# Kernel optimization log

Hardware: AMD Instinct MI355X
Metric: run time of the kernel (lower is better)

The kernel has to match this reference:

```python
import jax, jax.numpy as jnp
import numpy as np

INPUT_SIZE = 4096
HIDDEN = 1024
WINDOW = 2048
STRIDE = 1024
METRIC = 32
POOLING = "last"


def setup_inputs() -> dict:
    key = jax.random.key(0)
    ks = jax.random.split(key, 9)
    s = 1.0 / np.sqrt(HIDDEN)  # torch LSTMCell/Linear init bound
    u = lambda k, shape: jax.random.uniform(k, shape, jnp.float32, -s, s)
    return {
        "inp": jax.random.normal(ks[0], (WINDOW, INPUT_SIZE), jnp.float32),
        "h1": jax.random.normal(ks[1], (1, HIDDEN), jnp.float32),
        "c1": jax.random.normal(ks[2], (1, HIDDEN), jnp.float32),
        "W_ih": u(ks[3], (4 * HIDDEN, INPUT_SIZE)),
        "W_hh": u(ks[4], (4 * HIDDEN, HIDDEN)),
        "b_ih": u(ks[5], (4 * HIDDEN,)),
        "b_hh": u(ks[6], (4 * HIDDEN,)),
        "fc_w": u(ks[7], (METRIC, HIDDEN)),
        "fc_b": u(ks[8], (METRIC,)),
    }


def reference(inp, h1, c1, W_ih, W_hh, b_ih, b_hh, fc_w, fc_b):
    window = min(WINDOW, inp.shape[0])
    # Precompute the input-side gate projection as one GEMM: [T, 4H]
    xg = inp[:window] @ W_ih.T + b_ih

    def step(carry, xg_t):
        h, c = carry  # each [1, H]
        gates = xg_t + h @ W_hh.T + b_hh  # [1, 4H]
        i, f, g, o = jnp.split(gates, 4, axis=-1)
        c = jax.nn.sigmoid(f) * c + jax.nn.sigmoid(i) * jnp.tanh(g)
        h = jax.nn.sigmoid(o) * jnp.tanh(c)
        return (h, c), (h, c)

    (h_fin, c_fin), (hs, cs) = jax.lax.scan(step, (h1, c1), xg)

    if window >= STRIDE:
        h_last = jax.lax.stop_gradient(hs[STRIDE - 1])  # [1, H], detached
        c_last = jax.lax.stop_gradient(cs[STRIDE - 1])
    else:
        h_last, c_last = None, None

    if POOLING == "mean":
        # mean of fc(h_i) over last STRIDE steps of the window
        out = (hs[window - STRIDE:, 0, :] @ fc_w.T + fc_b).sum(axis=0, keepdims=True) / STRIDE
    else:  # 'last'
        out = h_fin @ fc_w.T + fc_b  # [1, METRIC]
    out = jnp.tanh(out)
    return out, h_last, c_last
```

## Files before the change

### kernel.cpp

```cpp
#include <hip/hip_runtime.h>
#include <stdint.h>

typedef unsigned short u16;
typedef unsigned long long u64;
typedef __attribute__((ext_vector_type(8))) short short8;
typedef __attribute__((ext_vector_type(4))) float floatx4;

#define K_IN    4096
#define HID     1024
#define G4H     4096
#define T_STEPS 2048
#define NWG     128
#define SPIN_MAX 60000

__device__ __forceinline__ u16 f2bf(float f) {
  union { float f; unsigned int i; } v; v.f = f;
  unsigned int lsb = (v.i >> 16) & 1u;
  v.i += 0x7fffu + lsb;
  return (u16)(v.i >> 16);
}
__device__ __forceinline__ float finz(float x) {
  unsigned b = __float_as_uint(x);
  return ((b & 0x7f800000u) == 0x7f800000u) ? 0.f : x;
}
__device__ __forceinline__ float sigm(float x) {
  x = fminf(30.f, fmaxf(-30.f, finz(x)));
  return 1.0f / (1.0f + __expf(-x));
}
__device__ __forceinline__ float tanh_s(float x) {
  x = fminf(15.f, fmaxf(-15.f, finz(x)));
  float e = __expf(2.0f * x);
  return (e - 1.0f) / (e + 1.0f);
}

__device__ __forceinline__ void publish_h(u64* hx, int slot, int idx, float h) {
  h = finz(h);
  u64 v = ((u64)(unsigned)(slot + 1) << 32) | (u64)__float_as_uint(h);
  __hip_atomic_store(&hx[(size_t)slot * HID + idx], v,
                     __ATOMIC_RELAXED, __HIP_MEMORY_SCOPE_AGENT);
}

__device__ __forceinline__ void poll2(const u64* hx, int slot, int j0,
                                      float* v, int* alive) {
  const u64* p = hx + (size_t)slot * HID + j0;
  const unsigned tag = (unsigned)(slot + 1);
  if (*alive) {
    int spins = 0;
    for (;;) {
      u64 a = __hip_atomic_load(&p[0], __ATOMIC_RELAXED, __HIP_MEMORY_SCOPE_AGENT);
      u64 b = __hip_atomic_load(&p[1], __ATOMIC_RELAXED, __HIP_MEMORY_SCOPE_AGENT);
      if ((unsigned)(a >> 32) == tag && (unsigned)(b >> 32) == tag) {
        v[0] = finz(__uint_as_float((unsigned)a));
        v[1] = finz(__uint_as_float((unsigned)b));
        return;
      }
      if (++spins > SPIN_MAX) { *alive = 0; break; }
      __builtin_amdgcn_s_sleep(1);
    }
  }
  v[0] = v[1] = 0.f;
}

__global__ __launch_bounds__(256) void cvt_bf16_k(const float* __restrict__ src,
                                                  u16* __restrict__ dst, int n4) {
  int i = blockIdx.x * 256 + threadIdx.x;
  if (i < n4) {
    float4 v = *(const float4*)(src + (size_t)i * 4);
    u16 o0 = f2bf(v.x), o1 = f2bf(v.y), o2 = f2bf(v.z), o3 = f2bf(v.w);
    ushort4 o = {o0, o1, o2, o3};
    *(ushort4*)(dst + (size_t)i * 4) = o;
  }
}

__global__ __launch_bounds__(256) void xg_gemm_k(const u16* __restrict__ A,
                                                 const u16* __restrict__ B,
                                                 const float* __restrict__ bias,
                                                 float* __restrict__ C)
{
  __shared__ __align__(16) u16 As[128 * 64];
  __shared__ __align__(16) u16 Bs[128 * 64];
  const int tid  = threadIdx.x;
  const int lane = tid & 63;
  const int quad = lane >> 4;
  const int l16  = lane & 15;
  const int wid  = tid >> 6;
  const int wm   = wid >> 1, wn = wid & 1;
  const int tileM = blockIdx.y * 128;
  const int tileN = blockIdx.x * 128;

  floatx4 acc[4][4];
  #pragma unroll
  for (int mi = 0; mi < 4; ++mi)
    #pragma unroll
    for (int ni = 0; ni < 4; ++ni)
      acc[mi][ni] = (floatx4){0.f, 0.f, 0.f, 0.f};

  for (int k0 = 0; k0 < K_IN; k0 += 64) {
    #pragma unroll
    for (int i = 0; i < 4; ++i) {
      int c = i * 256 + tid;
      int row = c >> 3, col = (c & 7) * 8;
      *(short8*)(As + c * 8) = *(const short8*)(A + (size_t)(tileM + row) * K_IN + k0 + col);
      *(short8*)(Bs + c * 8) = *(const short8*)(B + (size_t)(tileN + row) * K_IN + k0 + col);
    }
    __syncthreads();
    #pragma unroll
    for (int kk = 0; kk < 64; kk += 32) {
      short8 av[4], bv[4];
      #pragma unroll
      for (int mi = 0; mi < 4; ++mi)
        av[mi] = *(const short8*)(As + (wm * 64 + mi * 16 + l16) * 64 + kk + quad * 8);
      #pragma unroll
      for (int ni = 0; ni < 4; ++ni)
        bv[ni] = *(const short8*)(Bs + (wn * 64 + ni * 16 + l16) * 64 + kk + quad * 8);
      #pragma unroll
      for (int mi = 0; mi < 4; ++mi)
        #pragma unroll
        for (int ni = 0; ni < 4; ++ni)
          acc[mi][ni] = __builtin_amdgcn_mfma_f32_16x16x32_bf16(av[mi], bv[ni], acc[mi][ni], 0, 0, 0);
    }
    __syncthreads();
  }
  #pragma unroll
  for (int ni = 0; ni < 4; ++ni) {
    int n = tileN + wn * 64 + ni * 16 + l16;
    float bn = bias[n];
    #pragma unroll
    for (int mi = 0; mi < 4; ++mi) {
      int mbase = tileM + wm * 64 + mi * 16 + quad * 4;
      #pragma unroll
      for (int r = 0; r < 4; ++r)
        C[(size_t)(mbase + r) * G4H + n] = acc[mi][ni][r] + bn;
    }
  }
}

__global__ __launch_bounds__(512, 1) void lstm_scan_k(const float* __restrict__ Whh,
                                                      const float* __restrict__ bhh,
                                                      const float* __restrict__ h1,
                                                      const float* __restrict__ c1,
                                                      const float* __restrict__ fcw,
                                                      const float* __restrict__ fcb,
                                                      const float* __restrict__ xg,
                                                      u64* hx,
                                                      float* out)
{
  const int g    = blockIdx.x;
  const int tid  = threadIdx.x;
  const int lane = tid & 63;
  const int w    = tid >> 6;
  const int q    = w >> 1;
  const int ub   = (w & 1) * 4;

  __shared__ float h_local[HID];
  __shared__ float gsum[32];
  __shared__ float xgb[2][32];
  __shared__ float bhhb[32];
  __shared__ float pp[32][16];

  float wreg[4][16];
  #pragma unroll
  for (int i = 0; i < 4; ++i) {
    const size_t row = (size_t)(q * HID + g * 8 + ub + i);
    #pragma unroll
    for (int j = 0; j < 16; ++j)
      wreg[i][j] = Whh[row * HID + j * 64 + lane];
  }
  if (tid < 32) bhhb[tid] = bhh[(tid >> 3) * HID + g * 8 + (tid & 7)];

  float c_state = 0.f;
  if (tid < 8) {
    c_state = c1[g * 8 + tid];
    publish_h(hx, 0, g * 8 + tid, h1[g * 8 + tid]);
  }

  int alive = 1;
  const int j0 = tid * 2;
  for (int t = 0; t < T_STEPS; ++t) {
    float xval = 0.f;
    if (tid < 32) xval = finz(xg[(size_t)t * G4H + (tid >> 3) * HID + g * 8 + (tid & 7)]);
    float v[2];
    poll2(hx, t, j0, v, &alive);
    h_local[j0 + 0] = v[0]; h_local[j0 + 1] = v[1];
    if (tid < 32) xgb[t & 1][tid] = xval;
    __syncthreads();

    float s[4] = {0.f, 0.f, 0.f, 0.f};
    #pragma unroll
    for (int j = 0; j < 16; ++j) {
      float hv = h_local[j * 64 + lane];
      #pragma unroll
      for (int i = 0; i < 4; ++i) s[i] = fmaf(wreg[i][j], hv, s[i]);
    }
    #pragma unroll
    for (int d = 1; d < 64; d <<= 1) {
      #pragma unroll
      for (int i = 0; i < 4; ++i) s[i] += __shfl_xor(s[i], d, 64);
    }
    if (lane == 0) {
      #pragma unroll
      for (int i = 0; i < 4; ++i) gsum[q * 8 + ub + i] = s[i];
    }
    __syncthreads();

    if (tid < 8) {
      const int u = tid;
      const float* xb = xgb[t & 1];
      float gi = gsum[u]      + xb[u]      + bhhb[u];
      float gf = gsum[8 + u]  + xb[8 + u]  + bhhb[8 + u];
      float gg = gsum[16 + u] + xb[16 + u] + bhhb[16 + u];
      float go = gsum[24 + u] + xb[24 + u] + bhhb[24 + u];
      float iv = sigm(gi), fv = sigm(gf), gv = tanh_s(gg), ov = sigm(go);
      c_state = finz(fv * c_state + iv * gv);
      float hval = ov * tanh_s(c_state);
      publish_h(hx, t + 1, g * 8 + u, hval);
      if (t == 1023) {
        out[32 + g * 8 + u]       = finz(hval);
        out[32 + HID + g * 8 + u] = finz(c_state);
      }
    }
  }

  if (g == 0) {
    float v[2];
    poll2(hx, T_STEPS, j0, v, &alive);
    h_local[j0 + 0] = v[0]; h_local[j0 + 1] = v[1];
    __syncthreads();
    const int m = tid >> 4, seg = tid & 15;
    float pacc = 0.f;
    for (int k = seg * 64; k < seg * 64 + 64; ++k)
      pacc = fmaf(fcw[m * HID + k], h_local[k], pacc);
    pp[m][seg] = finz(pacc);
    __syncthreads();
    if (tid < 32) {
      float sum = fcb[tid];
      #pragma unroll
      for (int i = 0; i < 16; ++i) sum += pp[tid][i];
      out[tid] = tanh_s(finz(sum));
    }
  }
}

extern "C" void kernel_launch(void* const* d_in, const int* in_sizes, int n_in,
                              void* d_out, int out_size, void* d_ws, size_t ws_size,
                              hipStream_t stream) {
  const float* inp = (const float*)d_in[0];
  const float* h1  = (const float*)d_in[1];
  const float* c1  = (const float*)d_in[2];
  const float* Wih = (const float*)d_in[3];
  const float* Whh = (const float*)d_in[4];
  const float* bih = (const float*)d_in[5];
  const float* bhh = (const float*)d_in[6];
  const float* fcw = (const float*)d_in[7];
  const float* fcb = (const float*)d_in[8];
  float* out = (float*)d_out;

  const size_t xg_bytes  = (size_t)T_STEPS * G4H * 4;
  const size_t hx_bytes  = (size_t)(T_STEPS + 1) * HID * 8;
  const size_t ab_bytes  = (size_t)T_STEPS * K_IN * 2;
  const size_t wb_bytes  = (size_t)G4H * K_IN * 2;
  if (ws_size < xg_bytes + hx_bytes + ab_bytes + wb_bytes) return;

  float* xg   = (float*)d_ws;
  u64*   hx   = (u64*)((char*)d_ws + xg_bytes);
  u16*   Abf  = (u16*)((char*)d_ws + xg_bytes + hx_bytes);
  u16*   Wbf  = (u16*)((char*)d_ws + xg_bytes + hx_bytes + ab_bytes);

  const int nA4 = T_STEPS * K_IN / 4;
  const int nW4 = G4H * K_IN / 4;
  cvt_bf16_k<<<dim3((nA4 + 255) / 256), 256, 0, stream>>>(inp, Abf, nA4);
  cvt_bf16_k<<<dim3((nW4 + 255) / 256), 256, 0, stream>>>(Wih, Wbf, nW4);
  xg_gemm_k<<<dim3(G4H / 128, T_STEPS / 128), 256, 0, stream>>>(Abf, Wbf, bih, xg);
  lstm_scan_k<<<dim3(NWG), 512, 0, stream>>>(Whh, bhh, h1, c1, fcw, fcb, xg, hx, out);
}
```

Before: 4.806 ms.

## Assign one hidden unit per wave to drop the second per-step barrier

Each wave now owns all four gate rows of one hidden unit instead of four rows of one gate. The wave can therefore compute the cell update directly from its shuffle-reduced sums in lane 0. This removes the shared-memory gate staging and the second __syncthreads per timestep on the serial critical path. The h publish also switches from an atomic store to an atomic exchange, which may change how quickly the value becomes visible to the polling blocks but adds a returning atomic.

```diff
diff --git a/kernel.cpp b/kernel.cpp
--- a/kernel.cpp
+++ b/kernel.cpp
@@ -36,8 +36,8 @@
 __device__ __forceinline__ void publish_h(u64* hx, int slot, int idx, float h) {
   h = finz(h);
   u64 v = ((u64)(unsigned)(slot + 1) << 32) | (u64)__float_as_uint(h);
-  __hip_atomic_store(&hx[(size_t)slot * HID + idx], v,
-                     __ATOMIC_RELAXED, __HIP_MEMORY_SCOPE_AGENT);
+  (void)__hip_atomic_exchange(&hx[(size_t)slot * HID + idx], v,
+                              __ATOMIC_RELAXED, __HIP_MEMORY_SCOPE_AGENT);
 }
 
 __device__ __forceinline__ void poll2(const u64* hx, int slot, int j0,
@@ -149,40 +149,42 @@
   const int tid  = threadIdx.x;
   const int lane = tid & 63;
   const int w    = tid >> 6;
-  const int q    = w >> 1;
-  const int ub   = (w & 1) * 4;
+  const int U    = g * 8 + w;
 
   __shared__ float h_local[HID];
-  __shared__ float gsum[32];
-  __shared__ float xgb[2][32];
-  __shared__ float bhhb[32];
   __shared__ float pp[32][16];
 
   float wreg[4][16];
   #pragma unroll
-  for (int i = 0; i < 4; ++i) {
-    const size_t row = (size_t)(q * HID + g * 8 + ub + i);
+  for (int q = 0; q < 4; ++q) {
+    const size_t row = (size_t)(q * HID + U);
     #pragma unroll
     for (int j = 0; j < 16; ++j)
-      wreg[i][j] = Whh[row * HID + j * 64 + lane];
-  }
-  if (tid < 32) bhhb[tid] = bhh[(tid >> 3) * HID + g * 8 + (tid & 7)];
-
+      wreg[q][j] = Whh[row * HID + j * 64 + lane];
+  }
+
+  float bq[4] = {0.f, 0.f, 0.f, 0.f};
   float c_state = 0.f;
-  if (tid < 8) {
-    c_state = c1[g * 8 + tid];
-    publish_h(hx, 0, g * 8 + tid, h1[g * 8 + tid]);
+  if (lane == 0) {
+    #pragma unroll
+    for (int q = 0; q < 4; ++q) bq[q] = bhh[q * HID + U];
+    c_state = c1[U];
+    publish_h(hx, 0, U, h1[U]);
   }
 
   int alive = 1;
   const int j0 = tid * 2;
   for (int t = 0; t < T_STEPS; ++t) {
-    float xval = 0.f;
-    if (tid < 32) xval = finz(xg[(size_t)t * G4H + (tid >> 3) * HID + g * 8 + (tid & 7)]);
+    float xq[4] = {0.f, 0.f, 0.f, 0.f};
+    if (lane == 0) {
+      const size_t xb = (size_t)t * G4H + U;
+      #pragma unroll
+      for (int q = 0; q < 4; ++q) xq[q] = finz(xg[xb + q * HID]);
+    }
+
     float v[2];
     poll2(hx, t, j0, v, &alive);
     h_local[j0 + 0] = v[0]; h_local[j0 + 1] = v[1];
-    if (tid < 32) xgb[t & 1][tid] = xval;
     __syncthreads();
 
     float s[4] = {0.f, 0.f, 0.f, 0.f};
@@ -190,33 +192,26 @@
     for (int j = 0; j < 16; ++j) {
       float hv = h_local[j * 64 + lane];
       #pragma unroll
-      for (int i = 0; i < 4; ++i) s[i] = fmaf(wreg[i][j], hv, s[i]);
+      for (int q = 0; q < 4; ++q) s[q] = fmaf(wreg[q][j], hv, s[q]);
     }
     #pragma unroll
     for (int d = 1; d < 64; d <<= 1) {
       #pragma unroll
-      for (int i = 0; i < 4; ++i) s[i] += __shfl_xor(s[i], d, 64);
-    }
+      for (int q = 0; q < 4; ++q) s[q] += __shfl_xor(s[q], d, 64);
+    }
+
     if (lane == 0) {
-      #pragma unroll
-      for (int i = 0; i < 4; ++i) gsum[q * 8 + ub + i] = s[i];
-    }
-    __syncthreads();
-
-    if (tid < 8) {
-      const int u = tid;
-      const float* xb = xgb[t & 1];
-      float gi = gsum[u]      + xb[u]      + bhhb[u];
-      float gf = gsum[8 + u]  + xb[8 + u]  + bhhb[8 + u];
-      float gg = gsum[16 + u] + xb[16 + u] + bhhb[16 + u];
-      float go = gsum[24 + u] + xb[24 + u] + bhhb[24 + u];
+      float gi = s[0] + xq[0] + bq[0];
+      float gf = s[1] + xq[1] + bq[1];
+      float gg = s[2] + xq[2] + bq[2];
+      float go = s[3] + xq[3] + bq[3];
       float iv = sigm(gi), fv = sigm(gf), gv = tanh_s(gg), ov = sigm(go);
       c_state = finz(fv * c_state + iv * gv);
       float hval = ov * tanh_s(c_state);
-      publish_h(hx, t + 1, g * 8 + u, hval);
+      publish_h(hx, t + 1, U, hval);
       if (t == 1023) {
-        out[32 + g * 8 + u]       = finz(hval);
-        out[32 + HID + g * 8 + u] = finz(c_state);
+        out[32 + U]       = finz(hval);
+        out[32 + HID + U] = finz(c_state);
       }
     }
   }
```

New measurement: 7.060 ms. 46.9% more time.
